# Kernel tuning notes

Measured on AMD Instinct MI355X. Metric: run time of the kernel, lower is better.

## Reference

```python
import jax, jax.numpy as jnp
import numpy as np
import math

N = 50000        # nodes
DEG = 16         # regular out-degree -> E = N*DEG edges, grouped by source node
B = 64           # graphs in batch
F = 128          # num_node_features
H = 128          # nhid == enhid
RATIO = 0.5      # edge_ratio
NUM_CONVS = 3
E = N * DEG


def setup_inputs() -> dict:
    key = jax.random.key(0)
    ks = jax.random.split(key, 18)
    s = 0.05
    x = jax.random.normal(ks[0], (N, F), jnp.float32)
    edge_src = jnp.repeat(jnp.arange(N, dtype=jnp.int32), DEG)          # sorted by src
    edge_dst = jax.random.randint(ks[1], (E,), 0, N, jnp.int32)
    batch = ((jnp.arange(N) * B) // N).astype(jnp.int32)                 # sorted graph ids
    edge_attr = jnp.ones((E, 1), jnp.float32)                            # edge_attr=None branch
    inp = {"x": x, "edge_attr": edge_attr, "edge_src": edge_src,
           "edge_dst": edge_dst, "batch": batch}
    # GCNConv weights: [F->H, H->H, H->H]
    inp["W_gcn0"] = jax.random.normal(ks[2], (F, H), jnp.float32) * s
    inp["b_gcn0"] = jnp.zeros((H,), jnp.float32)
    inp["W_gcn1"] = jax.random.normal(ks[3], (H, H), jnp.float32) * s
    inp["b_gcn1"] = jnp.zeros((H,), jnp.float32)
    inp["W_gcn2"] = jax.random.normal(ks[4], (H, H), jnp.float32) * s
    inp["b_gcn2"] = jnp.zeros((H,), jnp.float32)
    # EGNN edge convs: [1->H, H->H]
    inp["W_eg0"] = jax.random.normal(ks[5], (1, H), jnp.float32) * s
    inp["b_eg0"] = jnp.zeros((H,), jnp.float32)
    inp["W_eg1"] = jax.random.normal(ks[6], (H, H), jnp.float32) * s
    inp["b_eg1"] = jnp.zeros((H,), jnp.float32)
    # score convs: [H->1, H->1]
    inp["W_sc0"] = jax.random.normal(ks[7], (H, 1), jnp.float32) * s
    inp["b_sc0"] = jnp.zeros((1,), jnp.float32)
    inp["W_sc1"] = jax.random.normal(ks[8], (H, 1), jnp.float32) * s
    inp["b_sc1"] = jnp.zeros((1,), jnp.float32)
    return inp


def _gcn(x, src, dst, ew, W, b):
    # PyG GCNConv: add self-loops (weight 1), symmetric deg normalization, aggregate at dst.
    n = x.shape[0]
    loop = jnp.arange(n, dtype=src.dtype)
    src2 = jnp.concatenate([src, loop])
    dst2 = jnp.concatenate([dst, loop])
    ew2 = jnp.concatenate([ew, jnp.ones((n,), ew.dtype)])
    deg = jax.ops.segment_sum(ew2, dst2, n)
    dinv = jnp.where(deg > 0, jax.lax.rsqrt(jnp.maximum(deg, 1e-12)), 0.0)
    norm = dinv[src2] * dinv[dst2] * ew2                                  # [E+n]
    msg = (x @ W)[src2] * norm[:, None]                                    # gather + scale
    return jax.ops.segment_sum(msg, dst2, n) + b                           # scatter-add


def _egnn(e, src, W, b):
    # Edge conv: scatter edge features to their source node, gather back, linear map.
    agg = jax.ops.segment_sum(e, src, N)
    return agg[src] @ W + b


def _pool(h, batch):
    gmax = jax.ops.segment_max(h, batch, B)
    gsum = jax.ops.segment_sum(h, batch, B)
    cnt = jax.ops.segment_sum(jnp.ones((h.shape[0],), h.dtype), batch, B)
    gmean = gsum / cnt[:, None]
    return jnp.concatenate([gmax, gmean, gsum], axis=1)                    # [B, 3H]


def reference(x, edge_attr, edge_src, edge_dst, batch,
              W_gcn0, b_gcn0, W_gcn1, b_gcn1, W_gcn2, b_gcn2,
              W_eg0, b_eg0, W_eg1, b_eg1, W_sc0, b_sc0, W_sc1, b_sc1):
    gW = [W_gcn0, W_gcn1, W_gcn2]
    gb = [b_gcn0, b_gcn1, b_gcn2]
    eW = [W_eg0, W_eg1]
    eb = [b_eg0, b_eg1]
    sW = [W_sc0, W_sc1]
    sb = [b_sc0, b_sc1]
    src, dst = edge_src, edge_dst
    deg = DEG
    ew = jnp.ones((src.shape[0],), jnp.float32)
    h = x
    ea = edge_attr
    xs = jnp.zeros((B, 3 * H), jnp.float32)
    for i in range(NUM_CONVS):
        h = jax.nn.relu(_gcn(h, src, dst, ew, gW[i], gb[i]))
        if i < NUM_CONVS - 1:
            ea = jax.nn.relu(_egnn(ea, src, eW[i], eb[i]))
            score = jnp.tanh(_egnn(ea, src, sW[i], sb[i])[:, 0])           # [E_cur]
            k = math.ceil(RATIO * deg)                                      # per-src-node top-k
            vals, idx = jax.lax.top_k(score.reshape(N, deg), k)             # [N,k]
            dst = jnp.take_along_axis(dst.reshape(N, deg), idx, axis=1).reshape(-1)
            flat = (jnp.arange(N)[:, None] * deg + idx).reshape(-1)
            ea = ea[flat]
            src = jnp.repeat(jnp.arange(N, dtype=src.dtype), k)
            ew = jnp.clip(vals.reshape(-1), 0.0, 1.0)
            deg = k
        xs = xs + _pool(h, batch)
    return xs
```

## Files before the change

### kernel.cpp

```cpp
#include <hip/hip_runtime.h>
#include <math.h>

#define NNODES 50000
#define DEGREE 16
#define NGRAPH 64
#define CAP 64
#define LDB 72
#define NXCD 8
#define XRANGE (NNODES / NXCD)
#define NTILE 782
#define ACHUNK 784
#define BCAP 192
#define NFILL 2048

typedef unsigned short u16;
typedef unsigned int u32;
typedef unsigned long long u64;
using short8 = __attribute__((ext_vector_type(8))) short;
using f32x4  = __attribute__((ext_vector_type(4))) float;
using fv4    = __attribute__((ext_vector_type(4))) float;

__device__ __forceinline__ u16 f2bf(float f) {
  union { float f; u32 u; } v; v.f = f;
  u32 u = v.u;
  return (u16)((u + 0x7FFFu + ((u >> 16) & 1u)) >> 16);
}
__device__ __forceinline__ float2 bf2x2(u32 u) {
  union { u32 u; float f; } lo, hi;
  lo.u = (u & 0xFFFFu) << 16; hi.u = u & 0xFFFF0000u;
  return make_float2(lo.f, hi.f);
}
__device__ __forceinline__ u32 pack2(float x, float y) {
  return (u32)f2bf(x) | ((u32)f2bf(y) << 16);
}
__device__ __forceinline__ int lowerb(const int* b, int n, int v) {
  int lo = 0, hi = n;
  while (lo < hi) { int m = (lo + hi) >> 1; if (b[m] < v) lo = m + 1; else hi = m; }
  return lo;
}

__device__ __forceinline__ void cons8(uint4 v, float w, float* acc) {
  float2 p;
  p = bf2x2(v.x); acc[0] = fmaf(w, p.x, acc[0]); acc[1] = fmaf(w, p.y, acc[1]);
  p = bf2x2(v.y); acc[2] = fmaf(w, p.x, acc[2]); acc[3] = fmaf(w, p.y, acc[3]);
  p = bf2x2(v.z); acc[4] = fmaf(w, p.x, acc[4]); acc[5] = fmaf(w, p.y, acc[5]);
  p = bf2x2(v.w); acc[6] = fmaf(w, p.x, acc[6]); acc[7] = fmaf(w, p.y, acc[7]);
}
__device__ __forceinline__ void consP(uint4 v, float* mx, float* sm) {
  float2 p;
  p = bf2x2(v.x);
  mx[0] = fmaxf(mx[0], p.x); sm[0] += p.x; mx[1] = fmaxf(mx[1], p.y); sm[1] += p.y;
  p = bf2x2(v.y);
  mx[2] = fmaxf(mx[2], p.x); sm[2] += p.x; mx[3] = fmaxf(mx[3], p.y); sm[3] += p.y;
  p = bf2x2(v.z);
  mx[4] = fmaxf(mx[4], p.x); sm[4] += p.x; mx[5] = fmaxf(mx[5], p.y); sm[5] += p.y;
  p = bf2x2(v.w);
  mx[6] = fmaxf(mx[6], p.x); sm[6] += p.x; mx[7] = fmaxf(mx[7], p.y); sm[7] += p.y;
}

__device__ __forceinline__ void pool_graph(
    int g, const u16* __restrict__ hpool, const int* __restrict__ batch,
    float* __restrict__ out, int poolAdd, float* P, int t) {
  int lane = t & 63;
  int wv = t >> 6;
  int q = lane >> 4, li = lane & 15;
  int lo = lowerb(batch, NNODES, g);
  int hi = lowerb(batch, NNODES, g + 1);
  const uint4* hb4 = reinterpret_cast<const uint4*>(hpool);
  float mx[8] = {0.f, 0.f, 0.f, 0.f, 0.f, 0.f, 0.f, 0.f};
  float sm[8] = {0.f, 0.f, 0.f, 0.f, 0.f, 0.f, 0.f, 0.f};
  int n = lo + wv * 4 + q;
  for (; n + 48 < hi; n += 64) {
    uint4 v0 = hb4[(size_t)n * 16 + li];
    uint4 v1 = hb4[(size_t)(n + 16) * 16 + li];
    uint4 v2 = hb4[(size_t)(n + 32) * 16 + li];
    uint4 v3 = hb4[(size_t)(n + 48) * 16 + li];
    consP(v0, mx, sm); consP(v1, mx, sm);
    consP(v2, mx, sm); consP(v3, mx, sm);
  }
  for (; n < hi; n += 16) {
    uint4 v = hb4[(size_t)n * 16 + li];
    consP(v, mx, sm);
  }
#pragma unroll
  for (int k = 0; k < 8; ++k) {
    mx[k] = fmaxf(mx[k], __shfl_xor(mx[k], 16, 64));
    mx[k] = fmaxf(mx[k], __shfl_xor(mx[k], 32, 64));
    sm[k] += __shfl_xor(sm[k], 16, 64);
    sm[k] += __shfl_xor(sm[k], 32, 64);
  }
  if (q == 0) {
#pragma unroll
    for (int k = 0; k < 8; ++k) {
      P[(wv * 16 + li) * 16 + k] = mx[k];
      P[(wv * 16 + li) * 16 + 8 + k] = sm[k];
    }
  }
  __syncthreads();
  if (t < 128) {
    int li2 = t >> 3, k = t & 7;
    int o0 = li2 * 16 + k, o1 = o0 + 8;
    float m = fmaxf(fmaxf(P[o0], P[256 + o0]),
                    fmaxf(P[512 + o0], P[768 + o0]));
    float s = P[o1] + P[256 + o1] + P[512 + o1] + P[768 + o1];
    float cf = (float)(hi - lo);
    int col = li2 * 8 + k;
    float* og = out + g * 384;
    if (poolAdd) {
      og[col] += m; og[128 + col] += s / cf; og[256 + col] += s;
    } else {
      og[col] = m;  og[128 + col] = s / cf;  og[256 + col] = s;
    }
  }
}

__global__ __launch_bounds__(256) void k_init(
    const float* __restrict__ eattr,
    const float* __restrict__ weg, const float* __restrict__ beg,
    const float* __restrict__ wsc, const float* __restrict__ bsc,
    const float* __restrict__ W0, const float* __restrict__ W1,
    const float* __restrict__ W2, const float* __restrict__ W3,
    float* __restrict__ ew1, float* __restrict__ agg0, u16* __restrict__ Wt,
    const int* __restrict__ edst, int* __restrict__ cnt,
    int* __restrict__ slots, int2* __restrict__ stag, int* __restrict__ scnt) {
  __shared__ int2 lbuf[NXCD * BCAP];
  __shared__ int lcnt[NXCD];
  int b = blockIdx.x, t = threadIdx.x;
  if (b < 196) {
    int i = b * 256 + t;
    if (i < NNODES) {
      const fv4* p = reinterpret_cast<const fv4*>(eattr + (size_t)i * DEGREE);
      float s = 0.f;
#pragma unroll
      for (int j = 0; j < 4; ++j) {
        fv4 w = __builtin_nontemporal_load(&p[j]);
        s += w.x + w.y + w.z + w.w;
      }
      agg0[i] = s;
      float sc = 0.f;
      for (int k = 0; k < 128; ++k) {
        float e = fmaxf(fmaf(s, weg[k], beg[k]), 0.f);
        sc = fmaf(e, wsc[k], sc);
      }
      float v1 = tanhf(fmaf(16.f, sc, bsc[0]));
      ew1[i] = fminf(fmaxf(v1, 0.f), 1.f);
    }
  } else if (b < 452) {
    int idx = (b - 196) * 256 + t;
    int which = idx >> 14, r = idx & 16383;
    int k = r >> 7, n = r & 127;
    const float* W = which == 0 ? W0 : which == 1 ? W1 : which == 2 ? W2 : W3;
    Wt[which * 16384 + n * 128 + k] = f2bf(W[k * 128 + n]);
  } else {
    int b2 = b - 452;
    if (t < NXCD) lcnt[t] = 0;
    __syncthreads();
    int e0 = b2 * ACHUNK;
    for (int k = 0; k < ACHUNK; k += 256) {
      int idx = k + t;
      int e = e0 + idx;
      if (idx < ACHUNK && e < NNODES * DEGREE) {
        int d = edst[e];
        u32 r = (u32)d / (u32)XRANGE;
        int pos = atomicAdd(&lcnt[r], 1);
        if (pos < BCAP) {
          lbuf[r * BCAP + pos] = make_int2(e, d);
        } else {
          int gp = atomicAdd(&cnt[d], 1);
          if (gp < CAP) slots[(size_t)d * CAP + gp] = e;
        }
      }
    }
    __syncthreads();
    for (int idx = t; idx < NXCD * BCAP; idx += 256) {
      int r = idx / BCAP, i = idx - r * BCAP;
      if (i < min(lcnt[r], BCAP))
        stag[((size_t)r * 1024 + b2) * BCAP + i] = lbuf[idx];
    }
    if (t < NXCD) scnt[t * 1024 + b2] = min(lcnt[t], BCAP);
  }
}

__global__ __launch_bounds__(256) void k_gemmF(
    int nFill, const int2* __restrict__ stag, const int* __restrict__ scnt,
    int* __restrict__ cnt, int* __restrict__ slots,
    int nGemm, const u16* __restrict__ A, const float* __restrict__ Af32,
    const u16* __restrict__ WtA, u16* __restrict__ outA,
    int nEg, const float* __restrict__ agg0, const float* __restrict__ weg,
    const float* __restrict__ beg, const u16* __restrict__ WtE,
    const float* __restrict__ beE, const float* __restrict__ wsc1,
    const float* __restrict__ bs1, float* __restrict__ ewOut,
    int nPool, const u16* __restrict__ hpool, const int* __restrict__ batch,
    float* __restrict__ out, int poolAdd) {
  __shared__ u16 Bs[128 * LDB];
  int b = blockIdx.x, t = threadIdx.x;
  int nWork = nGemm + nEg;
  int widx = 0, fidx = -1;
  if (nFill > 0) {
    if (b < 2 * nWork) { if (b & 1) fidx = b >> 1; else widx = b >> 1; }
    else fidx = nWork + (b - 2 * nWork);
  } else {
    if (nPool > 0 && b >= nWork) {
      pool_graph(b - nWork, hpool, batch, out, poolAdd,
                 reinterpret_cast<float*>(Bs), t);
      return;
    }
    widx = b;
  }
  if (fidx >= 0) {
    int r = fidx & (NXCD - 1), sub = fidx >> 3;
    int base[4]; int tot = 0;
#pragma unroll
    for (int q = 0; q < 4; ++q) {
      base[q] = tot;
      tot += scnt[r * 1024 + sub * 4 + q];
    }
    for (int idx = t; idx < tot; idx += 256) {
      int q = 0;
#pragma unroll
      for (int qq = 1; qq < 4; ++qq) if (idx >= base[qq]) q = qq;
      int i = idx - base[q];
      int2 v = stag[((size_t)r * 1024 + sub * 4 + q) * BCAP + i];
      int pos = atomicAdd(&cnt[v.y], 1);
      if (pos < CAP) slots[(size_t)v.y * CAP + pos] = v.x;
    }
    return;
  }
  int eg = (widx >= nGemm);
  const u16* Wsrc = eg ? WtE : WtA;
  int m0 = (eg ? (widx - nGemm) : widx) * 64;
  int wave = t >> 6, lane = t & 63;
  int lm = lane & 15, quad = lane >> 4;
  int row = m0 + wave * 16 + lm;
  short8 af[4];
  if (eg) {
    float a = (row < NNODES) ? agg0[row] : 0.f;
#pragma unroll
    for (int kc = 0; kc < 4; ++kc) {
      int k0 = kc * 32 + quad * 8;
      float v[8];
#pragma unroll
      for (int j = 0; j < 8; ++j)
        v[j] = 8.f * fmaxf(fmaf(a, weg[k0 + j], beg[k0 + j]), 0.f);
      uint4 o;
      o.x = pack2(v[0], v[1]); o.y = pack2(v[2], v[3]);
      o.z = pack2(v[4], v[5]); o.w = pack2(v[6], v[7]);
      af[kc] = *reinterpret_cast<short8*>(&o);
    }
  } else if (Af32) {
    if (row < NNODES) {
      const fv4* px = reinterpret_cast<const fv4*>(Af32 + (size_t)row * 128);
#pragma unroll
      for (int kc = 0; kc < 4; ++kc) {
        int k0 = (kc * 32 + quad * 8) >> 2;
        fv4 v0 = __builtin_nontemporal_load(&px[k0]);
        fv4 v1 = __builtin_nontemporal_load(&px[k0 + 1]);
        uint4 o;
        o.x = pack2(v0.x, v0.y); o.y = pack2(v0.z, v0.w);
        o.z = pack2(v1.x, v1.y); o.w = pack2(v1.z, v1.w);
        af[kc] = *reinterpret_cast<short8*>(&o);
      }
    } else {
      uint4 o = make_uint4(0u, 0u, 0u, 0u);
#pragma unroll
      for (int kc = 0; kc < 4; ++kc) af[kc] = *reinterpret_cast<short8*>(&o);
    }
  } else {
    if (row < NNODES) {
#pragma unroll
      for (int kc = 0; kc < 4; ++kc)
        af[kc] = *reinterpret_cast<const short8*>(
            &A[(size_t)row * 128 + kc * 32 + quad * 8]);
    } else {
      uint4 o = make_uint4(0u, 0u, 0u, 0u);
#pragma unroll
      for (int kc = 0; kc < 4; ++kc) af[kc] = *reinterpret_cast<short8*>(&o);
    }
  }
  f32x4 z = {0.f, 0.f, 0.f, 0.f};
  f32x4 acc[8];
#pragma unroll
  for (int n = 0; n < 8; ++n) acc[n] = z;
#pragma unroll
  for (int p = 0; p < 2; ++p) {
    if (p) __syncthreads();
    for (int i = t; i < 1024; i += 256) {
      int r = i >> 3, c = (i & 7) << 3;
      *reinterpret_cast<uint4*>(&Bs[r * LDB + c]) =
          *reinterpret_cast<const uint4*>(&Wsrc[r * 128 + p * 64 + c]);
    }
    __syncthreads();
#pragma unroll
    for (int kc2 = 0; kc2 < 2; ++kc2) {
      int kc = p * 2 + kc2;
#pragma unroll
      for (int n = 0; n < 8; ++n) {
        short8 bf = *reinterpret_cast<const short8*>(
            &Bs[(n * 16 + lm) * LDB + kc2 * 32 + quad * 8]);
        acc[n] = __builtin_amdgcn_mfma_f32_16x16x32_bf16(af[kc], bf, acc[n], 0, 0, 0);
      }
    }
  }
  if (!eg) {
#pragma unroll
    for (int n = 0; n < 8; ++n) {
      int col = n * 16 + lm;
#pragma unroll
      for (int r = 0; r < 4; ++r) {
        int orow = m0 + wave * 16 + quad * 4 + r;
        if (orow < NNODES) outA[(size_t)orow * 128 + col] = f2bf(acc[n][r]);
      }
    }
  } else {
    float s0 = 0.f, s1 = 0.f, s2 = 0.f, s3 = 0.f;
#pragma unroll
    for (int n = 0; n < 8; ++n) {
      int col = n * 16 + lm;
      float bb2 = beE[col], wv = wsc1[col];
      s0 = fmaf(fmaxf(acc[n][0] + bb2, 0.f), wv, s0);
      s1 = fmaf(fmaxf(acc[n][1] + bb2, 0.f), wv, s1);
      s2 = fmaf(fmaxf(acc[n][2] + bb2, 0.f), wv, s2);
      s3 = fmaf(fmaxf(acc[n][3] + bb2, 0.f), wv, s3);
    }
#pragma unroll
    for (int m = 8; m >= 1; m >>= 1) {
      s0 += __shfl_xor(s0, m, 64);
      s1 += __shfl_xor(s1, m, 64);
      s2 += __shfl_xor(s2, m, 64);
      s3 += __shfl_xor(s3, m, 64);
    }
    if (lm == 0) {
      float bsv = bs1[0];
      float sv[4] = {s0, s1, s2, s3};
#pragma unroll
      for (int r = 0; r < 4; ++r) {
        int orow = m0 + wave * 16 + quad * 4 + r;
        if (orow < NNODES) {
          float v = tanhf(fmaf(8.f, sv[r], bsv));
          ewOut[orow] = fminf(fmaxf(v, 0.f), 1.f);
        }
      }
    }
  }
}

template <int MODE>
__global__ __launch_bounds__(256) void k_agg(
    int nAgg, const u16* __restrict__ xwb, const int* __restrict__ cnt,
    const int* __restrict__ slots, const float* __restrict__ wsrc,
    const float* __restrict__ dinv, const float* __restrict__ bias,
    u16* __restrict__ hout,
    const u16* __restrict__ hpool, const int* __restrict__ batch,
    float* __restrict__ out,
    const float* __restrict__ ew1g, float* __restrict__ dv1,
    float* __restrict__ ws1,
    const float* __restrict__ ew2g, float* __restrict__ dv2,
    float* __restrict__ ws2) {
  constexpr int keep = (MODE == 0) ? 16 : (MODE == 1) ? 8 : 4;
  constexpr bool L0 = (MODE == 0);
  __shared__ float P[1024];
  int b = blockIdx.x, t = threadIdx.x;
  int lane = t & 63;
  int q = lane >> 4, li = lane & 15;
  if (b < nAgg) {
    int n = (b * 256 + t) >> 6;
    if (n >= NNODES) return;
    int c = min(cnt[n], CAP);
    u32 e = 0;
    if (lane < c) e = (u32)slots[(size_t)n * CAP + lane];
    if (L0) {
      u32 j = e & 15u; int srcn = (int)(e >> 4);
      float e1 = 0.f, e2 = 0.f;
      if (lane < c && j < 8u) {
        e1 = ew1g[srcn];
        if (j < 4u) e2 = ew2g[srcn];
      }
#pragma unroll
      for (int m = 32; m >= 1; m >>= 1) {
        e1 += __shfl_xor(e1, m, 64);
        e2 += __shfl_xor(e2, m, 64);
      }
      if (lane == 0) {
        float d1 = rsqrtf(1.0f + e1), d2 = rsqrtf(1.0f + e2);
        dv1[n] = d1; ws1[n] = d1 * ew1g[n];
        dv2[n] = d2; ws2[n] = d2 * ew2g[n];
      }
    }
    int kc; u32 ce;
    if (keep < 16) {
      bool valid = (lane < c) && ((e & 15u) < (u32)keep);
      u64 mask = __ballot(valid);
      kc = (int)__popcll(mask);
      u64 lt = ((u64)1 << lane) - 1;
      int pos = valid ? (int)__popcll(mask & lt) : 63 - (int)__popcll((~mask) & lt);
      ce = (u32)__builtin_amdgcn_ds_permute(pos << 2, (int)e);
    } else { kc = c; ce = e; }
    int sl = 0; float wl = 0.f;
    if (lane < kc) {
      sl = (int)(ce >> 4);
      wl = L0 ? rsqrtf(1.0f + (float)min(cnt[sl], CAP)) : wsrc[sl];
    }
    const uint4* b4 = reinterpret_cast<const uint4*>(xwb);
    uint4 selfv = b4[n * 16 + li];
    float acc[8] = {0.f, 0.f, 0.f, 0.f, 0.f, 0.f, 0.f, 0.f};
    for (int i = 0; i < kc; i += 16) {
      int r0 = i + q, r1 = i + 4 + q, r2 = i + 8 + q, r3 = i + 12 + q;
      int s0 = __shfl(sl, r0, 64); float w0 = __shfl(wl, r0, 64);
      int s1 = __shfl(sl, r1, 64); float w1 = __shfl(wl, r1, 64);
      int s2 = __shfl(sl, r2, 64); float w2 = __shfl(wl, r2, 64);
      int s3 = __shfl(sl, r3, 64); float w3 = __shfl(wl, r3, 64);
      if (r0 >= kc) { s0 = n; w0 = 0.f; }
      if (r1 >= kc) { s1 = n; w1 = 0.f; }
      if (r2 >= kc) { s2 = n; w2 = 0.f; }
      if (r3 >= kc) { s3 = n; w3 = 0.f; }
      uint4 v0 = b4[s0 * 16 + li];
      uint4 v1 = selfv, v2 = selfv, v3 = selfv;
      if (i + 4 < kc)  v1 = b4[s1 * 16 + li];
      if (i + 8 < kc)  v2 = b4[s2 * 16 + li];
      if (i + 12 < kc) v3 = b4[s3 * 16 + li];
      cons8(v0, w0, acc);
      cons8(v1, w1, acc);
      cons8(v2, w2, acc);
      cons8(v3, w3, acc);
    }
#pragma unroll
    for (int k = 0; k < 8; ++k) {
      acc[k] += __shfl_xor(acc[k], 16, 64);
      acc[k] += __shfl_xor(acc[k], 32, 64);
    }
    float di = L0 ? rsqrtf(1.0f + (float)c) : dinv[n];
    float dd = di * di;
    const f32x4* bp = reinterpret_cast<const f32x4*>(bias);
    f32x4 bv0 = bp[li * 2], bv1 = bp[li * 2 + 1];
    float2 p0 = bf2x2(selfv.x), p1 = bf2x2(selfv.y),
           p2 = bf2x2(selfv.z), p3 = bf2x2(selfv.w);
    float r0 = fmaxf(fmaf(di, acc[0], fmaf(dd, p0.x, bv0.x)), 0.f);
    float r1 = fmaxf(fmaf(di, acc[1], fmaf(dd, p0.y, bv0.y)), 0.f);
    float r2 = fmaxf(fmaf(di, acc[2], fmaf(dd, p1.x, bv0.z)), 0.f);
    float r3 = fmaxf(fmaf(di, acc[3], fmaf(dd, p1.y, bv0.w)), 0.f);
    float r4 = fmaxf(fmaf(di, acc[4], fmaf(dd, p2.x, bv1.x)), 0.f);
    float r5 = fmaxf(fmaf(di, acc[5], fmaf(dd, p2.y, bv1.y)), 0.f);
    float r6 = fmaxf(fmaf(di, acc[6], fmaf(dd, p3.x, bv1.z)), 0.f);
    float r7 = fmaxf(fmaf(di, acc[7], fmaf(dd, p3.y, bv1.w)), 0.f);
    if (q == 0) {
      uint4 o;
      o.x = pack2(r0, r1); o.y = pack2(r2, r3);
      o.z = pack2(r4, r5); o.w = pack2(r6, r7);
      reinterpret_cast<uint4*>(hout + (size_t)n * 128)[li] = o;
    }
  } else {
    pool_graph(b - nAgg, hpool, batch, out, 1, P, t);
  }
}

extern "C" void kernel_launch(void* const* d_in, const int* in_sizes, int n_in,
                              void* d_out, int out_size, void* d_ws, size_t ws_size,
                              hipStream_t stream) {
  const float* x     = (const float*)d_in[0];
  const float* eattr = (const float*)d_in[1];
  const int*   edst  = (const int*)d_in[3];
  const int*   batch = (const int*)d_in[4];
  const float* Wg0 = (const float*)d_in[5];  const float* bg0 = (const float*)d_in[6];
  const float* Wg1 = (const float*)d_in[7];  const float* bg1 = (const float*)d_in[8];
  const float* Wg2 = (const float*)d_in[9];  const float* bg2 = (const float*)d_in[10];
  const float* We0 = (const float*)d_in[11]; const float* be0 = (const float*)d_in[12];
  const float* We1 = (const float*)d_in[13]; const float* be1 = (const float*)d_in[14];
  const float* Ws0 = (const float*)d_in[15]; const float* bs0 = (const float*)d_in[16];
  const float* Ws1 = (const float*)d_in[17]; const float* bs1 = (const float*)d_in[18];
  float* out = (float*)d_out;

  char* ws = (char*)d_ws;
  const size_t NBH = (size_t)NNODES * 128 * 2;
  size_t off = 0;
  auto alloc = [&](size_t bytes) { void* p = ws + off; off = (off + bytes + 255) & ~(size_t)255; return p; };
  u16*   XWb   = (u16*)alloc(NBH);
  u16*   Hb0   = (u16*)alloc(NBH);
  u16*   Hb1   = (u16*)alloc(NBH);
  u16*   Hb2   = (u16*)alloc(NBH);
  u16*   Wtb   = (u16*)alloc(4 * 128 * 128 * 2);
  int*   slots = (int*)alloc((size_t)NNODES * CAP * 4);
  int*   cnt   = (int*)alloc((size_t)NNODES * 4);
  int2*  stag  = (int2*)alloc((size_t)NXCD * 1024 * BCAP * 8);
  int*   scnt  = (int*)alloc((size_t)NXCD * 1024 * 4);
  float* agg0  = (float*)alloc((size_t)NNODES * 4);
  float* ew1   = (float*)alloc((size_t)NNODES * 4);
  float* ew2   = (float*)alloc((size_t)NNODES * 4);
  float* dinv1 = (float*)alloc((size_t)NNODES * 4);
  float* wsrc1 = (float*)alloc((size_t)NNODES * 4);
  float* dinv2 = (float*)alloc((size_t)NNODES * 4);
  float* wsrc2 = (float*)alloc((size_t)NNODES * 4);

  hipMemsetAsync(cnt, 0, (size_t)NNODES * 4, stream);
  k_init<<<1476, 256, 0, stream>>>(eattr, We0, be0, Ws0, bs0,
                                   Wg0, Wg1, Wg2, We1, ew1, agg0, Wtb,
                                   edst, cnt, slots, stag, scnt);
  k_gemmF<<<2 * NTILE + NFILL, 256, 0, stream>>>(
      NFILL, stag, scnt, cnt, slots,
      NTILE, nullptr, x, Wtb, XWb,
      NTILE, agg0, We0, be0, Wtb + 3 * 16384, be1, Ws1, bs1, ew2,
      0, nullptr, nullptr, nullptr, 0);
  k_agg<0><<<12500, 256, 0, stream>>>(12500, XWb, cnt, slots, nullptr, nullptr,
                                      bg0, Hb0, nullptr, batch, nullptr,
                                      ew1, dinv1, wsrc1, ew2, dinv2, wsrc2);
  k_gemmF<<<NTILE + NGRAPH, 256, 0, stream>>>(
      0, nullptr, nullptr, nullptr, nullptr,
      NTILE, Hb0, nullptr, Wtb + 16384, XWb,
      0, nullptr, nullptr, nullptr, nullptr, nullptr, nullptr, nullptr, nullptr,
      NGRAPH, Hb0, batch, out, 0);
  k_agg<1><<<12500, 256, 0, stream>>>(12500, XWb, cnt, slots, wsrc1,
                                      dinv1, bg1, Hb1, nullptr, batch, out,
                                      nullptr, nullptr, nullptr,
                                      nullptr, nullptr, nullptr);
  k_gemmF<<<NTILE + NGRAPH, 256, 0, stream>>>(
      0, nullptr, nullptr, nullptr, nullptr,
      NTILE, Hb1, nullptr, Wtb + 2 * 16384, XWb,
      0, nullptr, nullptr, nullptr, nullptr, nullptr, nullptr, nullptr, nullptr,
      NGRAPH, Hb1, batch, out, 1);
  k_agg<2><<<12500, 256, 0, stream>>>(12500, XWb, cnt, slots, wsrc2,
                                      dinv2, bg2, Hb2, nullptr, batch, out,
                                      nullptr, nullptr, nullptr,
                                      nullptr, nullptr, nullptr);
  k_agg<3><<<NGRAPH, 256, 0, stream>>>(0, nullptr, cnt, slots, nullptr, nullptr,
                                       nullptr, nullptr, Hb2, batch, out,
                                       nullptr, nullptr, nullptr,
                                       nullptr, nullptr, nullptr);
}
```

Before: 284.4 us.

## Issue first weight tile load before A-fragment loads and double fill blocks

The GEMM path now starts staging the first half of the weight matrix into shared memory before it loads the A fragments. This lets the weight fetch latency overlap with the row loads instead of running after them. Separately, the number of fill blocks that drain the staged edge buckets into per-node slots is doubled, so each block handles two buckets instead of four. This gives more parallelism in the scatter phase, at the cost of more blocks and a changed bucket indexing that must match the producer side.

```diff
diff --git a/kernel.cpp b/kernel.cpp
--- a/kernel.cpp
+++ b/kernel.cpp
@@ -11,7 +11,7 @@
 #define NTILE 782
 #define ACHUNK 784
 #define BCAP 192
-#define NFILL 2048
+#define NFILL 4096
 
 typedef unsigned short u16;
 typedef unsigned int u32;
@@ -209,18 +209,12 @@
   }
   if (fidx >= 0) {
     int r = fidx & (NXCD - 1), sub = fidx >> 3;
-    int base[4]; int tot = 0;
-#pragma unroll
-    for (int q = 0; q < 4; ++q) {
-      base[q] = tot;
-      tot += scnt[r * 1024 + sub * 4 + q];
-    }
+    int base1 = scnt[r * 1024 + sub * 2];
+    int tot = base1 + scnt[r * 1024 + sub * 2 + 1];
     for (int idx = t; idx < tot; idx += 256) {
-      int q = 0;
-#pragma unroll
-      for (int qq = 1; qq < 4; ++qq) if (idx >= base[qq]) q = qq;
-      int i = idx - base[q];
-      int2 v = stag[((size_t)r * 1024 + sub * 4 + q) * BCAP + i];
+      int q = (idx >= base1) ? 1 : 0;
+      int i = idx - (q ? base1 : 0);
+      int2 v = stag[((size_t)r * 1024 + sub * 2 + q) * BCAP + i];
       int pos = atomicAdd(&cnt[v.y], 1);
       if (pos < CAP) slots[(size_t)v.y * CAP + pos] = v.x;
     }
@@ -232,6 +226,11 @@
   int wave = t >> 6, lane = t & 63;
   int lm = lane & 15, quad = lane >> 4;
   int row = m0 + wave * 16 + lm;
+  for (int i = t; i < 1024; i += 256) {
+    int r = i >> 3, c = (i & 7) << 3;
+    *reinterpret_cast<uint4*>(&Bs[r * LDB + c]) =
+        *reinterpret_cast<const uint4*>(&Wsrc[r * 128 + c]);
+  }
   short8 af[4];
   if (eg) {
     float a = (row < NNODES) ? agg0[row] : 0.f;
@@ -281,24 +280,30 @@
   f32x4 acc[8];
 #pragma unroll
   for (int n = 0; n < 8; ++n) acc[n] = z;
-#pragma unroll
-  for (int p = 0; p < 2; ++p) {
-    if (p) __syncthreads();
-    for (int i = t; i < 1024; i += 256) {
-      int r = i >> 3, c = (i & 7) << 3;
-      *reinterpret_cast<uint4*>(&Bs[r * LDB + c]) =
-          *reinterpret_cast<const uint4*>(&Wsrc[r * 128 + p * 64 + c]);
-    }
-    __syncthreads();
-#pragma unroll
-    for (int kc2 = 0; kc2 < 2; ++kc2) {
-      int kc = p * 2 + kc2;
-#pragma unroll
-      for (int n = 0; n < 8; ++n) {
-        short8 bf = *reinterpret_cast<const short8*>(
-            &Bs[(n * 16 + lm) * LDB + kc2 * 32 + quad * 8]);
-        acc[n] = __builtin_amdgcn_mfma_f32_16x16x32_bf16(af[kc], bf, acc[n], 0, 0, 0);
-      }
+  __syncthreads();
+#pragma unroll
+  for (int kc2 = 0; kc2 < 2; ++kc2) {
+#pragma unroll
+    for (int n = 0; n < 8; ++n) {
+      short8 bf = *reinterpret_cast<const short8*>(
+          &Bs[(n * 16 + lm) * LDB + kc2 * 32 + quad * 8]);
+      acc[n] = __builtin_amdgcn_mfma_f32_16x16x32_bf16(af[kc2], bf, acc[n], 0, 0, 0);
+    }
+  }
+  __syncthreads();
+  for (int i = t; i < 1024; i += 256) {
+    int r = i >> 3, c = (i & 7) << 3;
+    *reinterpret_cast<uint4*>(&Bs[r * LDB + c]) =
+        *reinterpret_cast<const uint4*>(&Wsrc[r * 128 + 64 + c]);
+  }
+  __syncthreads();
+#pragma unroll
+  for (int kc2 = 0; kc2 < 2; ++kc2) {
+#pragma unroll
+    for (int n = 0; n < 8; ++n) {
+      short8 bf = *reinterpret_cast<const short8*>(
+          &Bs[(n * 16 + lm) * LDB + kc2 * 32 + quad * 8]);
+      acc[n] = __builtin_amdgcn_mfma_f32_16x16x32_bf16(af[2 + kc2], bf, acc[n], 0, 0, 0);
     }
   }
   if (!eg) {
```

After: 282.0 us (median of 2 runs). No clear change (-0.8%).
